# Optimization experiments

Hardware: AMD Instinct MI355X
Metric: run time of the kernel (lower is better)

The kernel has to match this reference:

```python
import jax, jax.numpy as jnp
import numpy as np

ARITY = 4  # matches init_kwargs; params.shape[1] == 2**ARITY


def _high_order_act(X, params):
    # X: [B, G*arity], params: [G, 2**arity, O]
    B = X.shape[0]
    G, _, O = params.shape
    a = ARITY
    A = X.reshape(B, G, a)
    # sort ascending along the arity dim (torch.sort returns values + indices)
    A_ind = jnp.argsort(A, axis=2)                      # [B, G, a] int32
    A_sort = jnp.take_along_axis(A, A_ind, axis=2)      # [B, G, a]
    # barycentric-style coefficients: smallest value, then successive diffs
    coef = jnp.concatenate(
        [A_sort[:, :, :1], A_sort[:, :, 1:] - A_sort[:, :, :-1]], axis=2
    )                                                   # [B, G, a]
    # bit-power index: reverse cumsum of 2**A_ind -> suffix sums of bit masks
    pow2 = jnp.left_shift(jnp.int32(1), A_ind.astype(jnp.int32))  # [B, G, a]
    idx = jnp.cumsum(pow2[:, :, ::-1], axis=2)[:, :, ::-1]        # [B, G, a], in [1, 2**a - 1]
    # gather per-group table rows: params[g, idx[b,g,k], :]
    g_idx = jnp.arange(G)[None, :, None]                # [1, G, 1]
    gathered = params[g_idx, idx]                       # [B, G, a, O]
    # einsum 'jikl,ijk->ijl' in torch (j=G, i=B) == 'bgao,bga->bgo' here
    out = jnp.einsum('bgao,bga->bgo', gathered, coef)   # [B, G, O]
    return out.reshape(B, G * O)


def setup_inputs() -> dict:
    key = jax.random.key(0)
    kx, kp = jax.random.split(key)
    B, G, a, O = 8192, 256, ARITY, 16
    X = jax.random.normal(kx, (B, G * a), dtype=jnp.float32)
    params = jax.random.normal(kp, (G, 2 ** a, O), dtype=jnp.float32)
    return {"X": X, "params": params}


def reference(X, params):
    return _high_order_act(X, params)
```

## Files before the change

### kernel.cpp

```cpp
#include <hip/hip_runtime.h>


typedef float f32x4 __attribute__((ext_vector_type(4)));

#define TB 32
#define TG 16
#define TSTRIDE 260

__global__ __launch_bounds__(1024, 2) void hoa_kernel(
    const float* __restrict__ X, const float* __restrict__ P,
    float* __restrict__ out, int B, int G)
{
    __shared__ float lds[TG * TSTRIDE];

    const int tid = threadIdx.x;
    const int g0 = blockIdx.y * TG;
    const int b0 = blockIdx.x * TB;

    {
        int table = tid >> 6;
        int within = tid & 63;
        f32x4 v = *reinterpret_cast<const f32x4*>(
            P + (size_t)(g0 + table) * 256 + within * 4);
        *reinterpret_cast<f32x4*>(&lds[table * TSTRIDE + within * 4]) = v;
    }
    __syncthreads();

    const int c  = tid & 3;
    const int gg = (tid >> 2) & 15;
    const int bb = tid >> 6;
    const int g  = g0 + gg;
    const int b_lo = b0 + bb;
    const int b_hi = b_lo + 16;

    const float* tab = &lds[gg * TSTRIDE + c * 4];

    f32x4 x_pair[2];
    if (b_lo < B)
        x_pair[0] = __builtin_nontemporal_load(
            reinterpret_cast<const f32x4*>(X + (size_t)b_lo * (G * 4) + g * 4));
    if (b_hi < B)
        x_pair[1] = __builtin_nontemporal_load(
            reinterpret_cast<const f32x4*>(X + (size_t)b_hi * (G * 4) + g * 4));

#pragma unroll
    for (int r = 0; r < 2; ++r) {
        const int b = (r == 0) ? b_lo : b_hi;
        if (b >= B) continue;
        f32x4 x = x_pair[r];
        float v0 = x.x, v1 = x.y, v2 = x.z, v3 = x.w;
        int i0 = 0, i1 = 1, i2 = 2, i3 = 3;

#define CSWAP(va, vb, ia, ib)                         \
        {                                             \
            bool sw_ = (va) > (vb);                   \
            float lo_ = sw_ ? (vb) : (va);            \
            float hi_ = sw_ ? (va) : (vb);            \
            int il_ = sw_ ? (ib) : (ia);              \
            int ih_ = sw_ ? (ia) : (ib);              \
            (va) = lo_; (vb) = hi_; (ia) = il_; (ib) = ih_; \
        }
        CSWAP(v0, v1, i0, i1);
        CSWAP(v2, v3, i2, i3);
        CSWAP(v0, v2, i0, i2);
        CSWAP(v1, v3, i1, i3);
        CSWAP(v1, v2, i1, i2);
#undef CSWAP

        float c0 = v0, c1 = v1 - v0, c2 = v2 - v1, c3 = v3 - v2;
        int idx0 = 15;
        int idx1 = 15 ^ (1 << i0);
        int idx2 = idx1 ^ (1 << i1);
        int idx3 = 1 << i3;

        f32x4 A  = *reinterpret_cast<const f32x4*>(tab + idx0 * 16);
        f32x4 Bv = *reinterpret_cast<const f32x4*>(tab + idx1 * 16);
        f32x4 C  = *reinterpret_cast<const f32x4*>(tab + idx2 * 16);
        f32x4 D  = *reinterpret_cast<const f32x4*>(tab + idx3 * 16);

        f32x4 o;
        o.x = fmaf(c3, D.x, fmaf(c2, C.x, fmaf(c1, Bv.x, c0 * A.x)));
        o.y = fmaf(c3, D.y, fmaf(c2, C.y, fmaf(c1, Bv.y, c0 * A.y)));
        o.z = fmaf(c3, D.z, fmaf(c2, C.z, fmaf(c1, Bv.z, c0 * A.z)));
        o.w = fmaf(c3, D.w, fmaf(c2, C.w, fmaf(c1, Bv.w, c0 * A.w)));

        __builtin_nontemporal_store(
            o, reinterpret_cast<f32x4*>(out + (size_t)b * (G * 16) + g * 16 + c * 4));
    }
}

extern "C" void kernel_launch(void* const* d_in, const int* in_sizes, int n_in,
                              void* d_out, int out_size, void* d_ws, size_t ws_size,
                              hipStream_t stream) {
    const float* X = (const float*)d_in[0];
    const float* P = (const float*)d_in[1];
    float* out = (float*)d_out;

    int G = in_sizes[1] / 256;
    int B = in_sizes[0] / (G * 4);

    dim3 grid((B + TB - 1) / TB, G / TG);
    hipLaunchKernelGGL(hoa_kernel, grid, dim3(1024), 0, stream, X, P, out, B, G);
}
```

Before: 172.9 us.

## Process 64 rows per block with 512 threads and batched X loads

Shrinks the block to 512 threads and has each thread handle 8 batch rows instead of 2, so every block covers 64 rows. All 8 X vectors are loaded up front before any compute, giving more memory-level parallelism per thread. Each loaded 16-table LDS tile now serves four times as many rows, and there are fewer blocks and barriers. The cost is more registers per thread and fewer blocks to spread across the GPU.

```diff
diff --git a/kernel.cpp b/kernel.cpp
--- a/kernel.cpp
+++ b/kernel.cpp
@@ -3,11 +3,13 @@
 
 typedef float f32x4 __attribute__((ext_vector_type(4)));
 
-#define TB 32
+#define NT 512
 #define TG 16
+#define ROWS 64
+#define RPW 8
 #define TSTRIDE 260
 
-__global__ __launch_bounds__(1024, 2) void hoa_kernel(
+__global__ __launch_bounds__(NT, 4) void hoa_kernel(
     const float* __restrict__ X, const float* __restrict__ P,
     float* __restrict__ out, int B, int G)
 {
@@ -15,11 +17,13 @@
 
     const int tid = threadIdx.x;
     const int g0 = blockIdx.y * TG;
-    const int b0 = blockIdx.x * TB;
+    const int b0 = blockIdx.x * ROWS;
 
-    {
-        int table = tid >> 6;
-        int within = tid & 63;
+#pragma unroll
+    for (int i = 0; i < 2; ++i) {
+        int idx = tid + i * NT;
+        int table = idx >> 6;
+        int within = idx & 63;
         f32x4 v = *reinterpret_cast<const f32x4*>(
             P + (size_t)(g0 + table) * 256 + within * 4);
         *reinterpret_cast<f32x4*>(&lds[table * TSTRIDE + within * 4]) = v;
@@ -28,27 +32,27 @@
 
     const int c  = tid & 3;
     const int gg = (tid >> 2) & 15;
-    const int bb = tid >> 6;
+    const int wv = tid >> 6;
     const int g  = g0 + gg;
-    const int b_lo = b0 + bb;
-    const int b_hi = b_lo + 16;
 
     const float* tab = &lds[gg * TSTRIDE + c * 4];
+    const float* xp  = X   + (size_t)(b0 + wv) * (G * 4)  + g * 4;
+    float*       op  = out + (size_t)(b0 + wv) * (G * 16) + g * 16 + c * 4;
+    const size_t xstride = (size_t)RPW * G * 4;
+    const size_t ostride = (size_t)RPW * G * 16;
 
-    f32x4 x_pair[2];
-    if (b_lo < B)
-        x_pair[0] = __builtin_nontemporal_load(
-            reinterpret_cast<const f32x4*>(X + (size_t)b_lo * (G * 4) + g * 4));
-    if (b_hi < B)
-        x_pair[1] = __builtin_nontemporal_load(
-            reinterpret_cast<const f32x4*>(X + (size_t)b_hi * (G * 4) + g * 4));
+    f32x4 xs[RPW];
+#pragma unroll
+    for (int r = 0; r < RPW; ++r) {
+        if (b0 + wv + r * 8 < B)
+            xs[r] = __builtin_nontemporal_load(
+                reinterpret_cast<const f32x4*>(xp + r * xstride));
+    }
 
 #pragma unroll
-    for (int r = 0; r < 2; ++r) {
-        const int b = (r == 0) ? b_lo : b_hi;
-        if (b >= B) continue;
-        f32x4 x = x_pair[r];
-        float v0 = x.x, v1 = x.y, v2 = x.z, v3 = x.w;
+    for (int r = 0; r < RPW; ++r) {
+        if (b0 + wv + r * 8 >= B) continue;
+        float v0 = xs[r].x, v1 = xs[r].y, v2 = xs[r].z, v3 = xs[r].w;
         int i0 = 0, i1 = 1, i2 = 2, i3 = 3;
 
 #define CSWAP(va, vb, ia, ib)                         \
@@ -85,7 +89,7 @@
         o.w = fmaf(c3, D.w, fmaf(c2, C.w, fmaf(c1, Bv.w, c0 * A.w)));
 
         __builtin_nontemporal_store(
-            o, reinterpret_cast<f32x4*>(out + (size_t)b * (G * 16) + g * 16 + c * 4));
+            o, reinterpret_cast<f32x4*>(op + r * ostride));
     }
 }
 
@@ -99,6 +103,6 @@
     int G = in_sizes[1] / 256;
     int B = in_sizes[0] / (G * 4);
 
-    dim3 grid((B + TB - 1) / TB, G / TG);
-    hipLaunchKernelGGL(hoa_kernel, grid, dim3(1024), 0, stream, X, P, out, B, G);
+    dim3 grid((B + ROWS - 1) / ROWS, G / TG);
+    hipLaunchKernelGGL(hoa_kernel, grid, dim3(NT), 0, stream, X, P, out, B, G);
 }
```

After: 171.1 us. About the same (-1.0%).

## Drop LDS table staging and launch one block per batch row

Applied to the files above, without the earlier changes.

Replaces the 2D-tiled kernel, which staged 16 parameter tables into LDS per block, with a one-block-per-batch-row kernel that gathers table rows straight from global memory (relying on L1/L2 to hold the 256 KB params). This removes the LDS fill and the __syncthreads barrier, and gives fully contiguous row reads and writes. Nontemporal loads and stores are replaced with ordinary ones, and launch bounds are raised to request higher occupancy. The risk is that the scattered 16-byte table gathers now go to the cache hierarchy instead of LDS, and that ordinary stores may pollute L2.

```diff
diff --git a/kernel.cpp b/kernel.cpp
--- a/kernel.cpp
+++ b/kernel.cpp
@@ -3,51 +3,23 @@
 
 typedef float f32x4 __attribute__((ext_vector_type(4)));
 
-#define TB 32
-#define TG 16
-#define TSTRIDE 260
+#define NT 1024
 
-__global__ __launch_bounds__(1024, 2) void hoa_kernel(
+__global__ __launch_bounds__(NT, 8) void hoa_kernel(
     const float* __restrict__ X, const float* __restrict__ P,
     float* __restrict__ out, int B, int G)
 {
-    __shared__ float lds[TG * TSTRIDE];
+    const int b = blockIdx.x;
+    const int n = G * 4;
 
-    const int tid = threadIdx.x;
-    const int g0 = blockIdx.y * TG;
-    const int b0 = blockIdx.x * TB;
+    const float* xrow = X   + (size_t)b * n;
+    float*       orow = out + (size_t)b * (G * 16);
 
-    {
-        int table = tid >> 6;
-        int within = tid & 63;
-        f32x4 v = *reinterpret_cast<const f32x4*>(
-            P + (size_t)(g0 + table) * 256 + within * 4);
-        *reinterpret_cast<f32x4*>(&lds[table * TSTRIDE + within * 4]) = v;
-    }
-    __syncthreads();
+    for (int i = threadIdx.x; i < n; i += NT) {
+        const int c = i & 3;
+        const int g = i >> 2;
 
-    const int c  = tid & 3;
-    const int gg = (tid >> 2) & 15;
-    const int bb = tid >> 6;
-    const int g  = g0 + gg;
-    const int b_lo = b0 + bb;
-    const int b_hi = b_lo + 16;
-
-    const float* tab = &lds[gg * TSTRIDE + c * 4];
-
-    f32x4 x_pair[2];
-    if (b_lo < B)
-        x_pair[0] = __builtin_nontemporal_load(
-            reinterpret_cast<const f32x4*>(X + (size_t)b_lo * (G * 4) + g * 4));
-    if (b_hi < B)
-        x_pair[1] = __builtin_nontemporal_load(
-            reinterpret_cast<const f32x4*>(X + (size_t)b_hi * (G * 4) + g * 4));
-
-#pragma unroll
-    for (int r = 0; r < 2; ++r) {
-        const int b = (r == 0) ? b_lo : b_hi;
-        if (b >= B) continue;
-        f32x4 x = x_pair[r];
+        f32x4 x = *reinterpret_cast<const f32x4*>(xrow + g * 4);
         float v0 = x.x, v1 = x.y, v2 = x.z, v3 = x.w;
         int i0 = 0, i1 = 1, i2 = 2, i3 = 3;
 
@@ -73,10 +45,11 @@
         int idx2 = idx1 ^ (1 << i1);
         int idx3 = 1 << i3;
 
-        f32x4 A  = *reinterpret_cast<const f32x4*>(tab + idx0 * 16);
-        f32x4 Bv = *reinterpret_cast<const f32x4*>(tab + idx1 * 16);
-        f32x4 C  = *reinterpret_cast<const f32x4*>(tab + idx2 * 16);
-        f32x4 D  = *reinterpret_cast<const f32x4*>(tab + idx3 * 16);
+        const float* tp = P + (size_t)g * 256 + c * 4;
+        f32x4 A  = *reinterpret_cast<const f32x4*>(tp + idx0 * 16);
+        f32x4 Bv = *reinterpret_cast<const f32x4*>(tp + idx1 * 16);
+        f32x4 C  = *reinterpret_cast<const f32x4*>(tp + idx2 * 16);
+        f32x4 D  = *reinterpret_cast<const f32x4*>(tp + idx3 * 16);
 
         f32x4 o;
         o.x = fmaf(c3, D.x, fmaf(c2, C.x, fmaf(c1, Bv.x, c0 * A.x)));
@@ -84,8 +57,7 @@
         o.z = fmaf(c3, D.z, fmaf(c2, C.z, fmaf(c1, Bv.z, c0 * A.z)));
         o.w = fmaf(c3, D.w, fmaf(c2, C.w, fmaf(c1, Bv.w, c0 * A.w)));
 
-        __builtin_nontemporal_store(
-            o, reinterpret_cast<f32x4*>(out + (size_t)b * (G * 16) + g * 16 + c * 4));
+        *reinterpret_cast<f32x4*>(orow + i * 4) = o;
     }
 }
 
@@ -99,6 +71,5 @@
     int G = in_sizes[1] / 256;
     int B = in_sizes[0] / (G * 4);
 
-    dim3 grid((B + TB - 1) / TB, G / TG);
-    hipLaunchKernelGGL(hoa_kernel, grid, dim3(1024), 0, stream, X, P, out, B, G);
+    hipLaunchKernelGGL(hoa_kernel, dim3(B), dim3(NT), 0, stream, X, P, out, B, G);
 }
```

New measurement: 193.0 us. 11.6% more time.
